# Kernel tuning notes

Measured on AMD Instinct MI355X. Metric: run time of the kernel, lower is better.

Reference implementation:

```python
import jax, jax.numpy as jnp
import numpy as np
from jax import lax

DIM, GC1, GC2, GC3 = 128, 32, 64, 32
B, H, W = 4, 128, 128
EPS = 1e-5


def conv2d(x, w, b, pad, dilation=1, groups=1):
    y = lax.conv_general_dilated(x, w, (1, 1), [(pad, pad), (pad, pad)],
                                 rhs_dilation=(dilation, dilation),
                                 feature_group_count=groups,
                                 dimension_numbers=('NCHW', 'OIHW', 'NCHW'))
    return y + b[None, :, None, None]


def bilinear_gather(img, ys, xs):
    # img [B,C,H,W]; ys,xs [B,K,H,W] float sample coords. Zero padding outside.
    b, c, h, w = img.shape
    k = ys.shape[1]
    flat = img.reshape(b, c, h * w)
    y0 = jnp.floor(ys)
    x0 = jnp.floor(xs)
    acc = jnp.zeros((b, c, k, h, w), img.dtype)
    for dy in (0, 1):
        for dx in (0, 1):
            yc = y0 + dy
            xc = x0 + dx
            wgt = (1.0 - jnp.abs(ys - yc)) * (1.0 - jnp.abs(xs - xc))
            valid = (yc >= 0) & (yc <= h - 1) & (xc >= 0) & (xc <= w - 1)
            yi = jnp.clip(yc, 0, h - 1).astype(jnp.int32)
            xi = jnp.clip(xc, 0, w - 1).astype(jnp.int32)
            idx = (yi * w + xi).reshape(b, 1, k * h * w)
            g = jnp.take_along_axis(flat, jnp.broadcast_to(idx, (b, c, k * h * w)), axis=2)
            g = g.reshape(b, c, k, h, w)
            acc = acc + g * (wgt * valid.astype(img.dtype))[:, None]
    return acc


def deform_depthwise(x, off, w):
    # x [B,C,H,W], off [B,2*9,H,W] (dy,dx interleaved per kernel tap), w [C,9]
    b, c, h, ww = x.shape
    off = off.reshape(b, 9, 2, h, ww)
    dy, dx = off[:, :, 0], off[:, :, 1]  # [B,9,H,W]
    ks = jnp.arange(3, dtype=x.dtype)
    kyy = jnp.repeat(ks, 3)  # [9]
    kxx = jnp.tile(ks, 3)
    iy = jnp.arange(h, dtype=x.dtype)
    jx = jnp.arange(ww, dtype=x.dtype)
    ys = iy[None, None, :, None] - 1.0 + kyy[None, :, None, None] + dy
    xs = jx[None, None, None, :] - 1.0 + kxx[None, :, None, None] + dx
    sampled = bilinear_gather(x, ys, xs)  # [B,C,9,H,W]
    return jnp.einsum('bckhw,ck->bchw', sampled, w)


def batchnorm(x, g, b):
    mu = jnp.mean(x, axis=(0, 2, 3), keepdims=True)
    var = jnp.var(x, axis=(0, 2, 3), keepdims=True)
    return (x - mu) * lax.rsqrt(var + EPS) * g[None, :, None, None] + b[None, :, None, None]


def setup_inputs() -> dict:
    key = jax.random.key(0)
    ks = jax.random.split(key, 16)
    s = 0.05
    return {
        'x': jax.random.normal(ks[0], (B, DIM, H, W), jnp.float32),
        'offset_w': jax.random.normal(ks[1], (18, GC1, 3, 3), jnp.float32) * s,
        'offset_b': jax.random.normal(ks[2], (18,), jnp.float32) * s,
        'deform_w': jax.random.normal(ks[3], (GC1, 9), jnp.float32) * s,
        'dw_w': jax.random.normal(ks[4], (GC2, 1, 7, 7), jnp.float32) * s,
        'dw_b': jax.random.normal(ks[5], (GC2,), jnp.float32) * s,
        'dw2_w': jax.random.normal(ks[6], (GC3, GC3, 3, 3), jnp.float32) * s,
        'dw2_b': jax.random.normal(ks[7], (GC3,), jnp.float32) * s,
        'bn1_g': jnp.ones((DIM,), jnp.float32),
        'bn1_b': jnp.zeros((DIM,), jnp.float32),
        'w1': jax.random.normal(ks[8], (DIM, 4 * DIM), jnp.float32) * s,
        'b1': jax.random.normal(ks[9], (4 * DIM,), jnp.float32) * s,
        'w2': jax.random.normal(ks[10], (4 * DIM, DIM), jnp.float32) * s,
        'b2': jax.random.normal(ks[11], (DIM,), jnp.float32) * s,
        'bn2_g': jnp.ones((DIM,), jnp.float32),
        'bn2_b': jnp.zeros((DIM,), jnp.float32),
    }


def reference(x, offset_w, offset_b, deform_w, dw_w, dw_b, dw2_w, dw2_b,
              bn1_g, bn1_b, w1, b1, w2, b2, bn2_g, bn2_b):
    x_hw, x_w, x_h = jnp.split(x, [GC1, GC1 + GC2], axis=1)
    off = conv2d(x_hw, offset_w, offset_b, pad=1)
    d0 = deform_depthwise(x_hw, off, deform_w)
    d1 = conv2d(x_w, dw_w, dw_b, pad=3, groups=GC2)          # 7x7 depthwise
    d2 = conv2d(x_h, dw2_w, dw2_b, pad=2, dilation=2)        # 3x3 dense, dilation 2
    y = jnp.concatenate([d0, d1, d2], axis=1)
    # channel shuffle, groups=2
    b, c, h, w = y.shape
    y = y.reshape(b, 2, c // 2, h, w).transpose(0, 2, 1, 3, 4).reshape(b, c, h, w)
    y = batchnorm(y, bn1_g, bn1_b)
    t = y.transpose(0, 2, 3, 1)                               # [B,H,W,C]
    t = jax.nn.gelu(t @ w1 + b1, approximate=False)
    t = t @ w2 + b2
    y = t.transpose(0, 3, 1, 2)
    y = batchnorm(y, bn2_g, bn2_b)
    return jax.nn.gelu(x + y, approximate=False)
```

## Files before the change

### kernel.cpp

```cpp
#include <hip/hip_runtime.h>
#include <hip/hip_bf16.h>
#include <math.h>

#define BB 4
#define CC 128
#define HH 128
#define WWD 128
#define HWW 16384
#define PREC 17424

typedef __attribute__((ext_vector_type(8))) short bf16x8;
typedef __attribute__((ext_vector_type(4))) float floatx4;
typedef __attribute__((ext_vector_type(4))) unsigned short us4;
typedef __attribute__((ext_vector_type(8))) unsigned short us8;

__device__ __forceinline__ float gelu_fast(float v) {
  float u = v * v;
  float z = v * fmaf(0.0713548163f, u, 1.5957691216f);
  float e = __builtin_amdgcn_exp2f(-1.4426950409f * z);
  return v * __builtin_amdgcn_rcpf(1.0f + e);
}
__device__ __forceinline__ unsigned short f2us(float f) {
  union { float f; unsigned int u; } c; c.f = f;
  unsigned int u = c.u;
  return (unsigned short)((u + 0x7FFFu + ((u >> 16) & 1u)) >> 16);
}

__global__ __launch_bounds__(256) void k_zero(
    unsigned short* __restrict__ xp, float* __restrict__ part2) {
  if (blockIdx.x == 2178) { part2[threadIdx.x] = 0.f; return; }
  long i = ((long)blockIdx.x * 256 + threadIdx.x) * 8;
  us8 z = (us8)0;
  *(us8*)&xp[i] = z;
}

__global__ __launch_bounds__(256) void k_xt(
    const float* __restrict__ x, float* __restrict__ xt) {
  __shared__ float t[64 * 33];
  int bid = blockIdx.x;
  int tid = threadIdx.x;
  int b = bid >> 8, pg = bid & 255;
  int c = tid >> 3, g8 = tid & 7;
  const float* xp = x + ((long)b * CC + c) * HWW + pg * 64 + g8 * 8;
  float4 v0 = *(const float4*)xp;
  float4 v1 = *(const float4*)(xp + 4);
  t[(g8 * 8 + 0) * 33 + c] = v0.x; t[(g8 * 8 + 1) * 33 + c] = v0.y;
  t[(g8 * 8 + 2) * 33 + c] = v0.z; t[(g8 * 8 + 3) * 33 + c] = v0.w;
  t[(g8 * 8 + 4) * 33 + c] = v1.x; t[(g8 * 8 + 5) * 33 + c] = v1.y;
  t[(g8 * 8 + 6) * 33 + c] = v1.z; t[(g8 * 8 + 7) * 33 + c] = v1.w;
  __syncthreads();
  int u = tid >> 2, q = tid & 3;
  float4 o0, o1;
  o0.x = t[u * 33 + q * 8 + 0]; o0.y = t[u * 33 + q * 8 + 1];
  o0.z = t[u * 33 + q * 8 + 2]; o0.w = t[u * 33 + q * 8 + 3];
  o1.x = t[u * 33 + q * 8 + 4]; o1.y = t[u * 33 + q * 8 + 5];
  o1.z = t[u * 33 + q * 8 + 6]; o1.w = t[u * 33 + q * 8 + 7];
  float* d = xt + ((long)b * HWW + pg * 64 + u) * 32 + q * 8;
  *(float4*)d = o0;
  *(float4*)(d + 4) = o1;
}

__global__ __launch_bounds__(256) void k_pack(
    const float* __restrict__ x, unsigned short* __restrict__ xp) {
  __shared__ float t[64 * 33];
  int bid = blockIdx.x;
  int tid = threadIdx.x;
  int which = bid >> 10, b = (bid >> 8) & 3, pg = bid & 255;
  int cbase = which ? 96 : 0;
  int c = tid >> 3, g8 = tid & 7;
  const float* xpr = x + ((long)b * CC + cbase + c) * HWW + pg * 64 + g8 * 8;
  float4 v0 = *(const float4*)xpr;
  float4 v1 = *(const float4*)(xpr + 4);
  t[(g8 * 8 + 0) * 33 + c] = v0.x; t[(g8 * 8 + 1) * 33 + c] = v0.y;
  t[(g8 * 8 + 2) * 33 + c] = v0.z; t[(g8 * 8 + 3) * 33 + c] = v0.w;
  t[(g8 * 8 + 4) * 33 + c] = v1.x; t[(g8 * 8 + 5) * 33 + c] = v1.y;
  t[(g8 * 8 + 6) * 33 + c] = v1.z; t[(g8 * 8 + 7) * 33 + c] = v1.w;
  __syncthreads();
  int u = tid >> 2, q = tid & 3;
  int p = pg * 64 + u;
  int yy = p >> 7, xx = p & 127;
  long rec = (long)(which * 4 + b) * PREC + (yy + 2) * 132 + xx + 2;
  us8 o;
#pragma unroll
  for (int k = 0; k < 8; k++) o[k] = f2us(t[u * 33 + q * 8 + k]);
  *(us8*)&xp[rec * 32 + q * 8] = o;
}

__global__ __launch_bounds__(256) void k_wprep2(
    const float* __restrict__ offw, const float* __restrict__ dilw,
    unsigned short* __restrict__ wob, unsigned short* __restrict__ w3b) {
  int t = blockIdx.x * 256 + threadIdx.x;
  if (t >= 2304) return;
  int which = t >= 1152;
  int u = t - which * 1152;
  int lane = u & 63, tn = u >> 6;
  int col = lane & 15, quad = lane >> 4;
  int tap = tn >> 1, nt = tn & 1;
  int n = nt * 16 + col;
  const float* W = which ? dilw : offw;
  int noc = which ? 32 : 18;
  unsigned short* d = (which ? w3b : wob) + (long)(tn * 64 + lane) * 8;
#pragma unroll
  for (int j = 0; j < 8; j++)
    d[j] = (n < noc) ? f2us(W[(long)n * 288 + (quad * 8 + j) * 9 + tap]) : (unsigned short)0;
}

__global__ __launch_bounds__(256) void k_offc_mm(
    const unsigned short* __restrict__ xp0, const unsigned short* __restrict__ wob,
    const float* __restrict__ bias, float* __restrict__ off) {
  int bid = blockIdx.x;
  int b = bid >> 7, yy = bid & 127;
  int tid = threadIdx.x;
  int lane = tid & 63, wv = tid >> 6;
  int row = lane & 15, quad = lane >> 4;
  const unsigned short* plane = xp0 + (long)b * PREC * 32;
  int xb = wv * 32;
  floatx4 Oa[2][2];
#pragma unroll
  for (int mt = 0; mt < 2; mt++)
#pragma unroll
    for (int nt = 0; nt < 2; nt++) Oa[mt][nt] = (floatx4)0.f;
#pragma unroll
  for (int t = 0; t < 9; t++) {
    int dy = t / 3 - 1, dx = t % 3 - 1;
    const unsigned short* rp = plane + ((long)(yy + 2 + dy) * 132 + 2 + dx + xb) * 32;
    bf16x8 A0 = *(const bf16x8*)&rp[row * 32 + quad * 8];
    bf16x8 A1 = *(const bf16x8*)&rp[(16 + row) * 32 + quad * 8];
#pragma unroll
    for (int nt = 0; nt < 2; nt++) {
      bf16x8 Bf = *(const bf16x8*)&wob[(long)((t * 2 + nt) * 64 + lane) * 8];
      Oa[0][nt] = __builtin_amdgcn_mfma_f32_16x16x32_bf16(A0, Bf, Oa[0][nt], 0, 0, 0);
      Oa[1][nt] = __builtin_amdgcn_mfma_f32_16x16x32_bf16(A1, Bf, Oa[1][nt], 0, 0, 0);
    }
  }
#pragma unroll
  for (int nt = 0; nt < 2; nt++) {
    int oc = nt * 16 + (lane & 15);
    if (oc < 18) {
      float bb = bias[oc];
#pragma unroll
      for (int mt = 0; mt < 2; mt++) {
        floatx4 v = Oa[mt][nt];
        v[0] += bb; v[1] += bb; v[2] += bb; v[3] += bb;
        long p = (long)(b * 18 + oc) * HWW + yy * 128 + xb + mt * 16 + quad * 4;
        *(floatx4*)&off[p] = v;
      }
    }
  }
}

__global__ __launch_bounds__(256) void k_dil3_mm(
    const unsigned short* __restrict__ xp1, const unsigned short* __restrict__ w3b,
    const float* __restrict__ bias, float* __restrict__ y) {
  int bid = blockIdx.x;
  int b = bid >> 7, yy = bid & 127;
  int tid = threadIdx.x;
  int lane = tid & 63, wv = tid >> 6;
  int row = lane & 15, quad = lane >> 4;
  const unsigned short* plane = xp1 + (long)b * PREC * 32;
  int xb = wv * 32;
  floatx4 Oa[2][2];
#pragma unroll
  for (int mt = 0; mt < 2; mt++)
#pragma unroll
    for (int nt = 0; nt < 2; nt++) Oa[mt][nt] = (floatx4)0.f;
#pragma unroll
  for (int t = 0; t < 9; t++) {
    int dy = (t / 3 - 1) * 2, dx = (t % 3 - 1) * 2;
    const unsigned short* rp = plane + ((long)(yy + 2 + dy) * 132 + 2 + dx + xb) * 32;
    bf16x8 A0 = *(const bf16x8*)&rp[row * 32 + quad * 8];
    bf16x8 A1 = *(const bf16x8*)&rp[(16 + row) * 32 + quad * 8];
#pragma unroll
    for (int nt = 0; nt < 2; nt++) {
      bf16x8 Bf = *(const bf16x8*)&w3b[(long)((t * 2 + nt) * 64 + lane) * 8];
      Oa[0][nt] = __builtin_amdgcn_mfma_f32_16x16x32_bf16(A0, Bf, Oa[0][nt], 0, 0, 0);
      Oa[1][nt] = __builtin_amdgcn_mfma_f32_16x16x32_bf16(A1, Bf, Oa[1][nt], 0, 0, 0);
    }
  }
#pragma unroll
  for (int nt = 0; nt < 2; nt++) {
    int oc = nt * 16 + (lane & 15);
    int cp = 65 + 2 * oc;
    float bb = bias[oc];
#pragma unroll
    for (int mt = 0; mt < 2; mt++) {
      floatx4 v = Oa[mt][nt];
      v[0] += bb; v[1] += bb; v[2] += bb; v[3] += bb;
      long p = ((long)b * CC + cp) * HWW + yy * 128 + xb + mt * 16 + quad * 4;
      *(floatx4*)&y[p] = v;
    }
  }
}

__global__ __launch_bounds__(256) void k_deform(
    const float* __restrict__ xt, const float* __restrict__ off,
    const float* __restrict__ dw, float* __restrict__ y) {
  __shared__ float wl[144];
  int tid = threadIdx.x;
  int g = blockIdx.x * 256 + tid;
  int hf = g >> 16;
  int pix = g & 65535;
  if (tid < 144) {
    int k = tid >> 4, q = tid & 15;
    wl[k * 16 + q] = dw[(hf * 16 + q) * 9 + k];
  }
  __syncthreads();
  int b = pix >> 14, p = pix & 16383;
  int i = p >> 7, j = p & 127;
  float acc[16];
#pragma unroll
  for (int q = 0; q < 16; q++) acc[q] = 0.f;
  const float* offb = off + (long)b * 18 * HWW + p;
  const float* xb = xt + (long)b * HWW * 32 + hf * 16;
  for (int k = 0; k < 9; k++) {
    float dy = offb[(long)(2 * k) * HWW];
    float dx = offb[(long)(2 * k + 1) * HWW];
    float ys = (float)i - 1.f + (float)(k / 3) + dy;
    float xs = (float)j - 1.f + (float)(k % 3) + dx;
    float y0 = floorf(ys), x0 = floorf(xs);
    float fy = ys - y0, fx = xs - x0;
    int iy0 = (int)y0, ix0 = (int)x0;
    int iy1 = iy0 + 1, ix1 = ix0 + 1;
    float wy0 = (1.f - fy) * ((iy0 >= 0 && iy0 <= 127) ? 1.f : 0.f);
    float wy1 = fy * ((iy1 >= 0 && iy1 <= 127) ? 1.f : 0.f);
    float wx0 = (1.f - fx) * ((ix0 >= 0 && ix0 <= 127) ? 1.f : 0.f);
    float wx1 = fx * ((ix1 >= 0 && ix1 <= 127) ? 1.f : 0.f);
    int cy0 = min(max(iy0, 0), 127), cy1 = min(max(iy1, 0), 127);
    int cx0 = min(max(ix0, 0), 127), cx1 = min(max(ix1, 0), 127);
    int ci[4] = {cy0 * 128 + cx0, cy0 * 128 + cx1, cy1 * 128 + cx0, cy1 * 128 + cx1};
    float cw[4] = {wy0 * wx0, wy0 * wx1, wy1 * wx0, wy1 * wx1};
    float v[16];
#pragma unroll
    for (int q = 0; q < 16; q++) v[q] = 0.f;
#pragma unroll
    for (int cn = 0; cn < 4; cn++) {
      const float* cp = xb + (long)ci[cn] * 32;
      float wc = cw[cn];
      float4 p0 = *(const float4*)cp;
      float4 p1 = *(const float4*)(cp + 4);
      float4 p2 = *(const float4*)(cp + 8);
      float4 p3 = *(const float4*)(cp + 12);
      v[0] += wc * p0.x;  v[1] += wc * p0.y;  v[2] += wc * p0.z;  v[3] += wc * p0.w;
      v[4] += wc * p1.x;  v[5] += wc * p1.y;  v[6] += wc * p1.z;  v[7] += wc * p1.w;
      v[8] += wc * p2.x;  v[9] += wc * p2.y;  v[10] += wc * p2.z; v[11] += wc * p2.w;
      v[12] += wc * p3.x; v[13] += wc * p3.y; v[14] += wc * p3.z; v[15] += wc * p3.w;
    }
    const float* wr = &wl[k * 16];
#pragma unroll
    for (int q = 0; q < 16; q++) acc[q] += wr[q] * v[q];
  }
#pragma unroll
  for (int q = 0; q < 16; q++) {
    int cp = 2 * (hf * 16 + q);
    y[((long)b * CC + cp) * HWW + p] = acc[q];
  }
}

__global__ __launch_bounds__(256) void k_dw7(
    const float* __restrict__ x, const float* __restrict__ w,
    const float* __restrict__ bias, float* __restrict__ y) {
  __shared__ float tile[22 * 136];
  __shared__ float wl[49];
  __shared__ float bsh;
  int bid = blockIdx.x;
  int b = bid >> 9, m = (bid >> 3) & 63, strip = bid & 7;
  int r0 = strip * 16;
  int tid = threadIdx.x;
  const float* xp = x + ((long)b * CC + 32 + m) * HWW;
  for (int idx = tid; idx < 2948; idx += 256) {
    int rr = idx / 134;
    int cc = idx - rr * 134 - 3;
    int gy = r0 - 3 + rr;
    float v = 0.f;
    if ((unsigned)gy < 128u && (unsigned)cc < 128u) v = xp[gy * 128 + cc];
    tile[rr * 136 + cc + 3] = v;
  }
  if (tid < 49) wl[tid] = w[m * 49 + tid];
  if (tid == 64) bsh = bias[m];
  __syncthreads();
  int j = tid & 127, s = tid >> 7;
  float acc[8];
#pragma unroll
  for (int o = 0; o < 8; o++) acc[o] = bsh;
#pragma unroll
  for (int kx = 0; kx < 7; kx++) {
#pragma unroll
    for (int rr = 0; rr < 14; rr++) {
      float v = tile[(s * 8 + rr) * 136 + j + kx];
      int olo = rr - 6 > 0 ? rr - 6 : 0;
      int ohi = rr < 7 ? rr : 7;
#pragma unroll
      for (int o = 0; o < 8; o++) {
        if (o >= olo && o <= ohi) acc[o] += v * wl[(rr - o) * 7 + kx];
      }
    }
  }
  int c = 32 + m;
  int cp = (c & 63) * 2 + (c >> 6);
  float* yp = y + ((long)b * CC + cp) * HWW;
#pragma unroll
  for (int o = 0; o < 8; o++) {
    yp[(r0 + s * 8 + o) * 128 + j] = acc[o];
  }
}

__global__ __launch_bounds__(256) void k_stats1(
    const float* __restrict__ buf, float* __restrict__ part) {
  __shared__ float sh[256], sh2[256];
  int c = blockIdx.x >> 2, b = blockIdx.x & 3;
  int tid = threadIdx.x;
  const float* p = buf + ((long)b * CC + c) * HWW;
  float s = 0.f, s2 = 0.f;
  for (int it = 0; it < 16; it++) {
    float4 v = *(const float4*)(p + (it * 256 + tid) * 4);
    s += v.x + v.y + v.z + v.w;
    s2 += v.x * v.x + v.y * v.y + v.z * v.z + v.w * v.w;
  }
  sh[tid] = s; sh2[tid] = s2;
  __syncthreads();
  for (int o = 128; o > 0; o >>= 1) {
    if (tid < o) { sh[tid] += sh[tid + o]; sh2[tid] += sh2[tid + o]; }
    __syncthreads();
  }
  if (tid == 0) {
    part[blockIdx.x * 2] = sh[0];
    part[blockIdx.x * 2 + 1] = sh2[0];
  }
}

__global__ __launch_bounds__(128) void k_stats2(
    const float* __restrict__ part, float* __restrict__ mean, float* __restrict__ istd) {
  int c = threadIdx.x;
  float s = 0.f, s2 = 0.f;
#pragma unroll
  for (int b = 0; b < 4; b++) {
    s += part[(c * 4 + b) * 2];
    s2 += part[(c * 4 + b) * 2 + 1];
  }
  float mu = s * (1.f / 65536.f);
  float var = s2 * (1.f / 65536.f) - mu * mu;
  mean[c] = mu;
  istd[c] = rsqrtf(var + 1e-5f);
}

__global__ __launch_bounds__(128) void k_stats2b(
    const float* __restrict__ part2, float* __restrict__ mean, float* __restrict__ istd) {
  int c = threadIdx.x;
  float mu = part2[c] * (1.f / 65536.f);
  float var = part2[128 + c] * (1.f / 65536.f) - mu * mu;
  mean[c] = mu;
  istd[c] = rsqrtf(var + 1e-5f);
}

__global__ __launch_bounds__(256) void k_wprep(
    const float* __restrict__ w1, const float* __restrict__ w2,
    unsigned short* __restrict__ w1b, unsigned short* __restrict__ w2b) {
  int t = blockIdx.x * 256 + threadIdx.x;
  int which = t >> 13;
  int u = t & 8191;
  int lane = u & 63;
  int ntks = u >> 6;
  int col = lane & 15, quad = lane >> 4;
  if (which == 0) {
    int nt = ntks >> 2, ks = ntks & 3;
    int n = nt * 16 + col;
    int k0 = ks * 32 + quad * 8;
    unsigned short* d = w1b + (long)u * 8;
#pragma unroll
    for (int j = 0; j < 8; j++) d[j] = f2us(w1[(long)(k0 + j) * 512 + n]);
  } else {
    int nt = ntks >> 4, ks = ntks & 15;
    int n = nt * 16 + col;
    int k0 = ks * 32 + quad * 8;
    unsigned short* d = w2b + (long)u * 8;
#pragma unroll
    for (int j = 0; j < 8; j++) d[j] = f2us(w2[(long)(k0 + j) * 128 + n]);
  }
}

__global__ __launch_bounds__(256, 2) void k_mlp_mfma(
    const float* __restrict__ y, const float* __restrict__ mean1,
    const float* __restrict__ istd1, const float* __restrict__ g1,
    const float* __restrict__ b1n, const unsigned short* __restrict__ w1b,
    const float* __restrict__ b1, const unsigned short* __restrict__ w2b,
    const float* __restrict__ b2, float* __restrict__ tmid,
    float* __restrict__ part2) {
  __shared__ unsigned short At[128 * 136];
  __shared__ unsigned short Hs[4 * 32 * 72];
  __shared__ float scs[128], shs[128];
  __shared__ float ps[128], ps2[128];
  int tid = threadIdx.x;
  int lane = tid & 63, wv = tid >> 6;
  int row = lane & 15, quad = lane >> 4;
  int n0 = blockIdx.x * 128;
  int b = n0 >> 14;
  long base = (long)b * CC * HWW + (n0 & 16383);
  if (tid < 128) {
    float sc = istd1[tid] * g1[tid];
    scs[tid] = sc;
    shs[tid] = b1n[tid] - mean1[tid] * sc;
    ps[tid] = 0.f; ps2[tid] = 0.f;
  }
  __syncthreads();
  for (int it = 0; it < 16; it++) {
    int u = it * 256 + tid;
    int tok = u & 127, cg = u >> 7;
    us4 wvv;
#pragma unroll
    for (int r = 0; r < 4; r++) {
      int c = cg * 4 + r;
      float v = y[base + (long)c * HWW + tok];
      wvv[r] = f2us(v * scs[c] + shs[c]);
    }
    *(us4*)&At[tok * 136 + cg * 4] = wvv;
  }
  __syncthreads();
  bf16x8 Af[2][4];
#pragma unroll
  for (int mt = 0; mt < 2; mt++)
#pragma unroll
    for (int ks = 0; ks < 4; ks++)
      Af[mt][ks] = *(const bf16x8*)&At[(wv * 32 + mt * 16 + row) * 136 + ks * 32 + quad * 8];

  floatx4 Oa[2][8];
#pragma unroll
  for (int mt = 0; mt < 2; mt++)
#pragma unroll
    for (int nt = 0; nt < 8; nt++) Oa[mt][nt] = (floatx4)0.f;

  const int wvb = wv * 32 * 72;
  for (int ch = 0; ch < 8; ch++) {
    floatx4 Ha[4][2];
#pragma unroll
    for (int nt = 0; nt < 4; nt++)
#pragma unroll
      for (int mt = 0; mt < 2; mt++) Ha[nt][mt] = (floatx4)0.f;
#pragma unroll
    for (int nt = 0; nt < 4; nt++) {
      int ht = ch * 4 + nt;
#pragma unroll
      for (int ks = 0; ks < 4; ks++) {
        bf16x8 Wf = *(const bf16x8*)&w1b[(long)(((ht * 4 + ks) << 6) + lane) * 8];
        Ha[nt][0] = __builtin_amdgcn_mfma_f32_16x16x32_bf16(Wf, Af[0][ks], Ha[nt][0], 0, 0, 0);
        Ha[nt][1] = __builtin_amdgcn_mfma_f32_16x16x32_bf16(Wf, Af[1][ks], Ha[nt][1], 0, 0, 0);
      }
    }
#pragma unroll
    for (int nt = 0; nt < 4; nt++) {
      float4 bb = *(const float4*)&b1[ch * 64 + nt * 16 + quad * 4];
#pragma unroll
      for (int mt = 0; mt < 2; mt++) {
        us4 hv;
        hv[0] = f2us(gelu_fast(Ha[nt][mt][0] + bb.x));
        hv[1] = f2us(gelu_fast(Ha[nt][mt][1] + bb.y));
        hv[2] = f2us(gelu_fast(Ha[nt][mt][2] + bb.z));
        hv[3] = f2us(gelu_fast(Ha[nt][mt][3] + bb.w));
        *(us4*)&Hs[wvb + (mt * 16 + row) * 72 + nt * 16 + quad * 4] = hv;
      }
    }
    __syncthreads();
    bf16x8 A2[2][2];
#pragma unroll
    for (int mt = 0; mt < 2; mt++)
#pragma unroll
      for (int ks = 0; ks < 2; ks++)
        A2[mt][ks] = *(const bf16x8*)&Hs[wvb + (mt * 16 + row) * 72 + ks * 32 + quad * 8];
#pragma unroll
    for (int nt = 0; nt < 8; nt++) {
#pragma unroll
      for (int ks = 0; ks < 2; ks++) {
        bf16x8 Bf = *(const bf16x8*)&w2b[(long)(((nt * 16 + ch * 2 + ks) << 6) + lane) * 8];
        Oa[0][nt] = __builtin_amdgcn_mfma_f32_16x16x32_bf16(A2[0][ks], Bf, Oa[0][nt], 0, 0, 0);
        Oa[1][nt] = __builtin_amdgcn_mfma_f32_16x16x32_bf16(A2[1][ks], Bf, Oa[1][nt], 0, 0, 0);
      }
    }
    __syncthreads();
  }
#pragma unroll
  for (int nt = 0; nt < 8; nt++) {
    int c = nt * 16 + row;
    float bb = b2[c];
    long op = base + (long)c * HWW + wv * 32 + quad * 4;
    float s = 0.f, s2 = 0.f;
#pragma unroll
    for (int mt = 0; mt < 2; mt++) {
      floatx4 vv = Oa[mt][nt];
      vv[0] += bb; vv[1] += bb; vv[2] += bb; vv[3] += bb;
      *(floatx4*)&tmid[op + mt * 16] = vv;
      s += vv[0] + vv[1] + vv[2] + vv[3];
      s2 += vv[0] * vv[0] + vv[1] * vv[1] + vv[2] * vv[2] + vv[3] * vv[3];
    }
    atomicAdd(&ps[c], s);
    atomicAdd(&ps2[c], s2);
  }
  __syncthreads();
  if (tid < 128) {
    atomicAdd(&part2[tid], ps[tid]);
    atomicAdd(&part2[128 + tid], ps2[tid]);
  }
}

__global__ __launch_bounds__(256) void k_final(
    const float* __restrict__ x, const float* __restrict__ mean2,
    const float* __restrict__ istd2, const float* __restrict__ g2,
    const float* __restrict__ b2n, float* __restrict__ out) {
  long e4 = (long)blockIdx.x * 256 + threadIdx.x;
  int c = (int)((e4 >> 12) & 127);
  float sc = istd2[c] * g2[c];
  float sh = b2n[c] - mean2[c] * sc;
  float4 o = *(float4*)&out[e4 * 4];
  float4 xv = *(const float4*)&x[e4 * 4];
  o.x = gelu_fast(xv.x + o.x * sc + sh);
  o.y = gelu_fast(xv.y + o.y * sc + sh);
  o.z = gelu_fast(xv.z + o.z * sc + sh);
  o.w = gelu_fast(xv.w + o.w * sc + sh);
  *(float4*)&out[e4 * 4] = o;
}

extern "C" void kernel_launch(void* const* d_in, const int* in_sizes, int n_in,
                              void* d_out, int out_size, void* d_ws, size_t ws_size,
                              hipStream_t stream) {
  const float* x        = (const float*)d_in[0];
  const float* offset_w = (const float*)d_in[1];
  const float* offset_b = (const float*)d_in[2];
  const float* deform_w = (const float*)d_in[3];
  const float* dw_w     = (const float*)d_in[4];
  const float* dw_b     = (const float*)d_in[5];
  const float* dw2_w    = (const float*)d_in[6];
  const float* dw2_b    = (const float*)d_in[7];
  const float* bn1_g    = (const float*)d_in[8];
  const float* bn1_b    = (const float*)d_in[9];
  const float* w1       = (const float*)d_in[10];
  const float* b1       = (const float*)d_in[11];
  const float* w2       = (const float*)d_in[12];
  const float* b2       = (const float*)d_in[13];
  const float* bn2_g    = (const float*)d_in[14];
  const float* bn2_b    = (const float*)d_in[15];
  float* out = (float*)d_out;

  float* ws    = (float*)d_ws;
  float* off   = ws;
  float* ybuf  = ws + 1179648;
  float* stats = ws + 9568256;
  float* mean1 = stats, *istd1 = stats + 128;
  float* mean2 = stats + 256, *istd2 = stats + 384;
  unsigned short* w1b = (unsigned short*)(ws + 9568768);
  unsigned short* w2b = (unsigned short*)(ws + 9601536);
  float* part  = ws + 9634304;
  float* xt    = ws + 9635328;
  unsigned short* wob = (unsigned short*)(ws + 11732480);
  unsigned short* w3b = (unsigned short*)(ws + 11737088);
  unsigned short* xp  = (unsigned short*)(ws + 11741696);
  unsigned short* xp0 = xp;
  unsigned short* xp1 = xp + (long)4 * PREC * 32;
  float* part2 = ws + 13971968;
  float* tmid  = out;

  k_zero<<<2179, 256, 0, stream>>>(xp, part2);
  k_wprep<<<64, 256, 0, stream>>>(w1, w2, w1b, w2b);
  k_wprep2<<<9, 256, 0, stream>>>(offset_w, dw2_w, wob, w3b);
  k_pack<<<2048, 256, 0, stream>>>(x, xp);
  k_xt<<<1024, 256, 0, stream>>>(x, xt);
  k_offc_mm<<<512, 256, 0, stream>>>(xp0, wob, offset_b, off);
  k_deform<<<512, 256, 0, stream>>>(xt, off, deform_w, ybuf);
  k_dw7<<<2048, 256, 0, stream>>>(x, dw_w, dw_b, ybuf);
  k_dil3_mm<<<512, 256, 0, stream>>>(xp1, w3b, dw2_b, ybuf);
  k_stats1<<<512, 256, 0, stream>>>(ybuf, part);
  k_stats2<<<1, 128, 0, stream>>>(part, mean1, istd1);
  k_mlp_mfma<<<512, 256, 0, stream>>>(ybuf, mean1, istd1, bn1_g, bn1_b, w1b, b1, w2b, b2, tmid, part2);
  k_stats2b<<<1, 128, 0, stream>>>(part2, mean2, istd2);
  k_final<<<8192, 256, 0, stream>>>(x, mean2, istd2, bn2_g, bn2_b, out);
}
```

Before: 279.7 us.

## Halve MLP token tile per block and alias hidden buffer into input LDS

The fused MLP kernel now handles 64 tokens per block instead of 128, with each wave owning 16 token rows, and launches twice as many blocks. The GELU hidden tile is written into the wave's own slice of the input LDS tile, so the separate Hs array is gone. Together with fewer accumulator registers, this lowers per-block LDS and VGPR use so launch bounds can request 4 blocks per SIMD. The aim is higher occupancy and better latency hiding. The trade-off is that each weight fragment loaded from memory now feeds one MFMA instead of two, which doubles weight traffic through L2.

```diff
diff --git a/kernel.cpp b/kernel.cpp
--- a/kernel.cpp
+++ b/kernel.cpp
@@ -378,21 +378,20 @@
   }
 }
 
-__global__ __launch_bounds__(256, 2) void k_mlp_mfma(
+__global__ __launch_bounds__(256, 4) void k_mlp_mfma(
     const float* __restrict__ y, const float* __restrict__ mean1,
     const float* __restrict__ istd1, const float* __restrict__ g1,
     const float* __restrict__ b1n, const unsigned short* __restrict__ w1b,
     const float* __restrict__ b1, const unsigned short* __restrict__ w2b,
     const float* __restrict__ b2, float* __restrict__ tmid,
     float* __restrict__ part2) {
-  __shared__ unsigned short At[128 * 136];
-  __shared__ unsigned short Hs[4 * 32 * 72];
+  __shared__ unsigned short At[64 * 136];
   __shared__ float scs[128], shs[128];
   __shared__ float ps[128], ps2[128];
   int tid = threadIdx.x;
   int lane = tid & 63, wv = tid >> 6;
   int row = lane & 15, quad = lane >> 4;
-  int n0 = blockIdx.x * 128;
+  int n0 = blockIdx.x * 64;
   int b = n0 >> 14;
   long base = (long)b * CC * HWW + (n0 & 16383);
   if (tid < 128) {
@@ -402,9 +401,9 @@
     ps[tid] = 0.f; ps2[tid] = 0.f;
   }
   __syncthreads();
-  for (int it = 0; it < 16; it++) {
+  for (int it = 0; it < 8; it++) {
     int u = it * 256 + tid;
-    int tok = u & 127, cg = u >> 7;
+    int tok = u & 63, cg = u >> 6;
     us4 wvv;
 #pragma unroll
     for (int r = 0; r < 4; r++) {
@@ -415,63 +414,50 @@
     *(us4*)&At[tok * 136 + cg * 4] = wvv;
   }
   __syncthreads();
-  bf16x8 Af[2][4];
-#pragma unroll
-  for (int mt = 0; mt < 2; mt++)
-#pragma unroll
-    for (int ks = 0; ks < 4; ks++)
-      Af[mt][ks] = *(const bf16x8*)&At[(wv * 32 + mt * 16 + row) * 136 + ks * 32 + quad * 8];
-
-  floatx4 Oa[2][8];
-#pragma unroll
-  for (int mt = 0; mt < 2; mt++)
-#pragma unroll
-    for (int nt = 0; nt < 8; nt++) Oa[mt][nt] = (floatx4)0.f;
-
-  const int wvb = wv * 32 * 72;
+  bf16x8 Af[4];
+#pragma unroll
+  for (int ks = 0; ks < 4; ks++)
+    Af[ks] = *(const bf16x8*)&At[(wv * 16 + row) * 136 + ks * 32 + quad * 8];
+  unsigned short* HsW = &At[wv * 16 * 136];
+
+  floatx4 Oa[8];
+#pragma unroll
+  for (int nt = 0; nt < 8; nt++) Oa[nt] = (floatx4)0.f;
+
   for (int ch = 0; ch < 8; ch++) {
-    floatx4 Ha[4][2];
-#pragma unroll
-    for (int nt = 0; nt < 4; nt++)
-#pragma unroll
-      for (int mt = 0; mt < 2; mt++) Ha[nt][mt] = (floatx4)0.f;
+    floatx4 Ha[4];
+#pragma unroll
+    for (int nt = 0; nt < 4; nt++) Ha[nt] = (floatx4)0.f;
 #pragma unroll
     for (int nt = 0; nt < 4; nt++) {
       int ht = ch * 4 + nt;
 #pragma unroll
       for (int ks = 0; ks < 4; ks++) {
         bf16x8 Wf = *(const bf16x8*)&w1b[(long)(((ht * 4 + ks) << 6) + lane) * 8];
-        Ha[nt][0] = __builtin_amdgcn_mfma_f32_16x16x32_bf16(Wf, Af[0][ks], Ha[nt][0], 0, 0, 0);
-        Ha[nt][1] = __builtin_amdgcn_mfma_f32_16x16x32_bf16(Wf, Af[1][ks], Ha[nt][1], 0, 0, 0);
+        Ha[nt] = __builtin_amdgcn_mfma_f32_16x16x32_bf16(Wf, Af[ks], Ha[nt], 0, 0, 0);
       }
     }
 #pragma unroll
     for (int nt = 0; nt < 4; nt++) {
       float4 bb = *(const float4*)&b1[ch * 64 + nt * 16 + quad * 4];
-#pragma unroll
-      for (int mt = 0; mt < 2; mt++) {
-        us4 hv;
-        hv[0] = f2us(gelu_fast(Ha[nt][mt][0] + bb.x));
-        hv[1] = f2us(gelu_fast(Ha[nt][mt][1] + bb.y));
-        hv[2] = f2us(gelu_fast(Ha[nt][mt][2] + bb.z));
-        hv[3] = f2us(gelu_fast(Ha[nt][mt][3] + bb.w));
-        *(us4*)&Hs[wvb + (mt * 16 + row) * 72 + nt * 16 + quad * 4] = hv;
-      }
+      us4 hv;
+      hv[0] = f2us(gelu_fast(Ha[nt][0] + bb.x));
+      hv[1] = f2us(gelu_fast(Ha[nt][1] + bb.y));
+      hv[2] = f2us(gelu_fast(Ha[nt][2] + bb.z));
+      hv[3] = f2us(gelu_fast(Ha[nt][3] + bb.w));
+      *(us4*)&HsW[row * 72 + nt * 16 + quad * 4] = hv;
     }
     __syncthreads();
-    bf16x8 A2[2][2];
-#pragma unroll
-    for (int mt = 0; mt < 2; mt++)
-#pragma unroll
-      for (int ks = 0; ks < 2; ks++)
-        A2[mt][ks] = *(const bf16x8*)&Hs[wvb + (mt * 16 + row) * 72 + ks * 32 + quad * 8];
+    bf16x8 A2[2];
+#pragma unroll
+    for (int ks = 0; ks < 2; ks++)
+      A2[ks] = *(const bf16x8*)&HsW[row * 72 + ks * 32 + quad * 8];
 #pragma unroll
     for (int nt = 0; nt < 8; nt++) {
 #pragma unroll
       for (int ks = 0; ks < 2; ks++) {
         bf16x8 Bf = *(const bf16x8*)&w2b[(long)(((nt * 16 + ch * 2 + ks) << 6) + lane) * 8];
-        Oa[0][nt] = __builtin_amdgcn_mfma_f32_16x16x32_bf16(A2[0][ks], Bf, Oa[0][nt], 0, 0, 0);
-        Oa[1][nt] = __builtin_amdgcn_mfma_f32_16x16x32_bf16(A2[1][ks], Bf, Oa[1][nt], 0, 0, 0);
+        Oa[nt] = __builtin_amdgcn_mfma_f32_16x16x32_bf16(A2[ks], Bf, Oa[nt], 0, 0, 0);
       }
     }
     __syncthreads();
@@ -480,16 +466,12 @@
   for (int nt = 0; nt < 8; nt++) {
     int c = nt * 16 + row;
     float bb = b2[c];
-    long op = base + (long)c * HWW + wv * 32 + quad * 4;
-    float s = 0.f, s2 = 0.f;
-#pragma unroll
-    for (int mt = 0; mt < 2; mt++) {
-      floatx4 vv = Oa[mt][nt];
-      vv[0] += bb; vv[1] += bb; vv[2] += bb; vv[3] += bb;
-      *(floatx4*)&tmid[op + mt * 16] = vv;
-      s += vv[0] + vv[1] + vv[2] + vv[3];
-      s2 += vv[0] * vv[0] + vv[1] * vv[1] + vv[2] * vv[2] + vv[3] * vv[3];
-    }
+    long op = base + (long)c * HWW + wv * 16 + quad * 4;
+    floatx4 vv = Oa[nt];
+    vv[0] += bb; vv[1] += bb; vv[2] += bb; vv[3] += bb;
+    *(floatx4*)&tmid[op] = vv;
+    float s = vv[0] + vv[1] + vv[2] + vv[3];
+    float s2 = vv[0] * vv[0] + vv[1] * vv[1] + vv[2] * vv[2] + vv[3] * vv[3];
     atomicAdd(&ps[c], s);
     atomicAdd(&ps2[c], s2);
   }
@@ -567,7 +549,7 @@
   k_dil3_mm<<<512, 256, 0, stream>>>(xp1, w3b, dw2_b, ybuf);
   k_stats1<<<512, 256, 0, stream>>>(ybuf, part);
   k_stats2<<<1, 128, 0, stream>>>(part, mean1, istd1);
-  k_mlp_mfma<<<512, 256, 0, stream>>>(ybuf, mean1, istd1, bn1_g, bn1_b, w1b, b1, w2b, b2, tmid, part2);
+  k_mlp_mfma<<<1024, 256, 0, stream>>>(ybuf, mean1, istd1, bn1_g, bn1_b, w1b, b1, w2b, b2, tmid, part2);
   k_stats2b<<<1, 128, 0, stream>>>(part2, mean2, istd2);
   k_final<<<8192, 256, 0, stream>>>(x, mean2, istd2, bn2_g, bn2_b, out);
 }
```

After: 294.8 us. +5.4%, slower.

## Feed GELU hidden activations directly from MFMA registers into second GEMM

Applied to the files above, without the earlier changes.

Reorders the K dimension of the packed second-layer weights so that each lane's first-GEMM accumulator outputs line up with the A-operand fragment of the second GEMM. The hidden activations then stay in registers instead of going through a shared-memory Hs buffer, which drops the LDS write, one barrier and the LDS read per chunk. This frees shared memory and may help occupancy. It relies on the weight-permutation being exactly consistent with the MFMA register layout.

```diff
diff --git a/kernel.cpp b/kernel.cpp
--- a/kernel.cpp
+++ b/kernel.cpp
@@ -371,10 +371,13 @@
   } else {
     int nt = ntks >> 4, ks = ntks & 15;
     int n = nt * 16 + col;
-    int k0 = ks * 32 + quad * 8;
+    int ch = ks >> 1, sfl = ks & 1;
     unsigned short* d = w2b + (long)u * 8;
 #pragma unroll
-    for (int j = 0; j < 8; j++) d[j] = f2us(w2[(long)(k0 + j) * 128 + n]);
+    for (int j = 0; j < 8; j++) {
+      int h = ch * 64 + (2 * sfl + (j >> 2)) * 16 + quad * 4 + (j & 3);
+      d[j] = f2us(w2[(long)h * 128 + n]);
+    }
   }
 }
 
@@ -386,7 +389,6 @@
     const float* __restrict__ b2, float* __restrict__ tmid,
     float* __restrict__ part2) {
   __shared__ unsigned short At[128 * 136];
-  __shared__ unsigned short Hs[4 * 32 * 72];
   __shared__ float scs[128], shs[128];
   __shared__ float ps[128], ps2[128];
   int tid = threadIdx.x;
@@ -428,7 +430,6 @@
 #pragma unroll
     for (int nt = 0; nt < 8; nt++) Oa[mt][nt] = (floatx4)0.f;
 
-  const int wvb = wv * 32 * 72;
   for (int ch = 0; ch < 8; ch++) {
     floatx4 Ha[4][2];
 #pragma unroll
@@ -445,33 +446,32 @@
         Ha[nt][1] = __builtin_amdgcn_mfma_f32_16x16x32_bf16(Wf, Af[1][ks], Ha[nt][1], 0, 0, 0);
       }
     }
-#pragma unroll
-    for (int nt = 0; nt < 4; nt++) {
-      float4 bb = *(const float4*)&b1[ch * 64 + nt * 16 + quad * 4];
+    bf16x8 Hf[2][2];
+#pragma unroll
+    for (int s = 0; s < 2; s++) {
+      float4 bbA = *(const float4*)&b1[ch * 64 + (2 * s) * 16 + quad * 4];
+      float4 bbB = *(const float4*)&b1[ch * 64 + (2 * s + 1) * 16 + quad * 4];
 #pragma unroll
       for (int mt = 0; mt < 2; mt++) {
-        us4 hv;
-        hv[0] = f2us(gelu_fast(Ha[nt][mt][0] + bb.x));
-        hv[1] = f2us(gelu_fast(Ha[nt][mt][1] + bb.y));
-        hv[2] = f2us(gelu_fast(Ha[nt][mt][2] + bb.z));
-        hv[3] = f2us(gelu_fast(Ha[nt][mt][3] + bb.w));
-        *(us4*)&Hs[wvb + (mt * 16 + row) * 72 + nt * 16 + quad * 4] = hv;
+        us8 hv;
+        hv[0] = f2us(gelu_fast(Ha[2 * s][mt][0] + bbA.x));
+        hv[1] = f2us(gelu_fast(Ha[2 * s][mt][1] + bbA.y));
+        hv[2] = f2us(gelu_fast(Ha[2 * s][mt][2] + bbA.z));
+        hv[3] = f2us(gelu_fast(Ha[2 * s][mt][3] + bbA.w));
+        hv[4] = f2us(gelu_fast(Ha[2 * s + 1][mt][0] + bbB.x));
+        hv[5] = f2us(gelu_fast(Ha[2 * s + 1][mt][1] + bbB.y));
+        hv[6] = f2us(gelu_fast(Ha[2 * s + 1][mt][2] + bbB.z));
+        hv[7] = f2us(gelu_fast(Ha[2 * s + 1][mt][3] + bbB.w));
+        Hf[s][mt] = *(bf16x8*)&hv;
       }
     }
-    __syncthreads();
-    bf16x8 A2[2][2];
-#pragma unroll
-    for (int mt = 0; mt < 2; mt++)
-#pragma unroll
-      for (int ks = 0; ks < 2; ks++)
-        A2[mt][ks] = *(const bf16x8*)&Hs[wvb + (mt * 16 + row) * 72 + ks * 32 + quad * 8];
 #pragma unroll
     for (int nt = 0; nt < 8; nt++) {
 #pragma unroll
-      for (int ks = 0; ks < 2; ks++) {
-        bf16x8 Bf = *(const bf16x8*)&w2b[(long)(((nt * 16 + ch * 2 + ks) << 6) + lane) * 8];
-        Oa[0][nt] = __builtin_amdgcn_mfma_f32_16x16x32_bf16(A2[0][ks], Bf, Oa[0][nt], 0, 0, 0);
-        Oa[1][nt] = __builtin_amdgcn_mfma_f32_16x16x32_bf16(A2[1][ks], Bf, Oa[1][nt], 0, 0, 0);
+      for (int s = 0; s < 2; s++) {
+        bf16x8 Bf = *(const bf16x8*)&w2b[(long)(((nt * 16 + ch * 2 + s) << 6) + lane) * 8];
+        Oa[0][nt] = __builtin_amdgcn_mfma_f32_16x16x32_bf16(Hf[s][0], Bf, Oa[0][nt], 0, 0, 0);
+        Oa[1][nt] = __builtin_amdgcn_mfma_f32_16x16x32_bf16(Hf[s][1], Bf, Oa[1][nt], 0, 0, 0);
       }
     }
     __syncthreads();
```

Measured after the change: 300.4 us. 7.4% more time.
